# Kernel optimization log

Hardware: AMD Instinct MI355X
Metric: run time of the kernel (lower is better)

The kernel has to match this reference:

```python
import jax, jax.numpy as jnp
import numpy as np

U_NUM = 100000
I_NUM = 50000
D = 64
E = 4_000_000
N_LAYERS = 3


def setup_inputs() -> dict:
    key = jax.random.key(0)
    k1, k2, k3, k4 = jax.random.split(key, 4)
    return {
        "user_emb": jax.random.normal(k1, (U_NUM + 1, D), dtype=jnp.float32) * 0.1,
        "item_emb": jax.random.normal(k2, (I_NUM + 1, D), dtype=jnp.float32) * 0.1,
        "edge_user": jax.random.randint(k3, (E,), 0, U_NUM + 1, dtype=jnp.int32),
        "edge_item": jax.random.randint(k4, (E,), 0, I_NUM + 1, dtype=jnp.int32),
    }


def reference(user_emb, item_emb, edge_user, edge_item):
    U = user_emb.shape[0]
    I = item_emb.shape[0]
    N = U + I
    # Symmetrize bipartite interaction edges into full-graph COO indices.
    rows = jnp.concatenate([edge_user, edge_item + U])          # [2E]
    cols = jnp.concatenate([edge_item + U, edge_user])          # [2E]
    # Symmetric degree normalization: A_hat = D^-1/2 A D^-1/2 (deg + 1e-7)
    deg = jax.ops.segment_sum(jnp.ones(rows.shape[0], dtype=jnp.float32), rows, num_segments=N) + 1e-7
    d_inv_sqrt = deg ** -0.5
    vals = d_inv_sqrt[rows] * d_inv_sqrt[cols]                  # [2E]

    emb = jnp.concatenate([user_emb, item_emb], axis=0)         # [N, D]
    acc = emb
    x = emb
    for _ in range(N_LAYERS):
        # SpMM: x_new[r] = sum_{edges (r,c)} vals * x[c]
        x = jax.ops.segment_sum(vals[:, None] * x[cols], rows, num_segments=N)
        acc = acc + x
    total = acc / jnp.float32(N_LAYERS + 1)                     # mean over layer stack
    return total[:U], total[U:]
```

## Files before the change

### kernel.cpp

```cpp
#include <hip/hip_runtime.h>


static constexpr int D = 64;
#define BSHIFT 8
#define BROWS 256
#define KP 1024
#define TILE 4096
#define TK 16
#define PADSLACK (7 * BROWS)
#define FULL_CAP 16384
#define COLS_SLACK 8192

__device__ __forceinline__ float bflo(unsigned v) {
    unsigned u = v << 16;
    return __builtin_bit_cast(float, u);
}
__device__ __forceinline__ float bfhi(unsigned v) {
    unsigned u = v & 0xFFFF0000u;
    return __builtin_bit_cast(float, u);
}
__device__ __forceinline__ unsigned pack_bf16x2(float a, float b) {
    unsigned ua = __builtin_bit_cast(unsigned, a);
    unsigned ub = __builtin_bit_cast(unsigned, b);
    ua += 0x7FFFu + ((ua >> 16) & 1u);
    ub += 0x7FFFu + ((ub >> 16) & 1u);
    return (ua >> 16) | (ub & 0xFFFF0000u);
}
__device__ __forceinline__ unsigned pack_f16x2(float a, float b) {
    unsigned short ua = __builtin_bit_cast(unsigned short, (_Float16)a);
    unsigned short ub = __builtin_bit_cast(unsigned short, (_Float16)b);
    return (unsigned)ua | ((unsigned)ub << 16);
}
__device__ __forceinline__ float f16lo(unsigned v) {
    return (float)__builtin_bit_cast(_Float16, (unsigned short)(v & 0xFFFFu));
}
__device__ __forceinline__ float f16hi(unsigned v) {
    return (float)__builtin_bit_cast(_Float16, (unsigned short)(v >> 16));
}

__device__ __forceinline__ void acc_bf2(unsigned u, float& se, float& so) {
    se += bflo(u);
    so += bfhi(u);
}

__global__ __launch_bounds__(256) void bucket_count(
        const int* __restrict__ eu, const int* __restrict__ ei,
        int* __restrict__ bcnt, int E, int U) {
    __shared__ int h[KP];
    int tid = threadIdx.x;
#pragma unroll
    for (int k = 0; k < 4; ++k) h[tid + k * 256] = 0;
    __syncthreads();
    int E4 = E >> 2;
    int stride = gridDim.x * blockDim.x;
    int g = blockIdx.x * blockDim.x + tid;
    const int4* eu4 = (const int4*)eu;
    const int4* ei4 = (const int4*)ei;
    for (int e = g; e < E4; e += stride) {
        int4 u = eu4[e];
        int4 it = ei4[e];
        atomicAdd(&h[u.x >> BSHIFT], 1);
        atomicAdd(&h[u.y >> BSHIFT], 1);
        atomicAdd(&h[u.z >> BSHIFT], 1);
        atomicAdd(&h[u.w >> BSHIFT], 1);
        atomicAdd(&h[(U + it.x) >> BSHIFT], 1);
        atomicAdd(&h[(U + it.y) >> BSHIFT], 1);
        atomicAdd(&h[(U + it.z) >> BSHIFT], 1);
        atomicAdd(&h[(U + it.w) >> BSHIFT], 1);
    }
    if (blockIdx.x == 0 && tid < (E - (E4 << 2))) {
        int e = (E4 << 2) + tid;
        atomicAdd(&h[eu[e] >> BSHIFT], 1);
        atomicAdd(&h[(U + ei[e]) >> BSHIFT], 1);
    }
    __syncthreads();
#pragma unroll
    for (int k = 0; k < 4; ++k) {
        int v = h[tid + k * 256];
        if (v) atomicAdd(&bcnt[tid + k * 256], v);
    }
}

__global__ void bscan(const int* __restrict__ bcnt, int* __restrict__ bbase,
                      int* __restrict__ bcursor, int KB, int twoE) {
    __shared__ int s[KP];
    int tid = threadIdx.x;
    int v = (tid < KB) ? bcnt[tid] : 0;
    s[tid] = v;
    __syncthreads();
    for (int off = 1; off < KP; off <<= 1) {
        int a = (tid >= off) ? s[tid - off] : 0;
        __syncthreads();
        s[tid] += a;
        __syncthreads();
    }
    int ex = s[tid] - v;
    if (tid < KB) { bbase[tid] = ex; bcursor[tid] = ex; }
    if (tid == KB) bbase[tid] = twoE;
    if (tid > KB) bcursor[tid] = 0;
}

__global__ __launch_bounds__(256) void bucket_scatter(
        const int* __restrict__ eu, const int* __restrict__ ei,
        int* __restrict__ bcursor, unsigned* __restrict__ pairs,
        int E, int U, int twoE) {
    __shared__ int hist[KP];
    __shared__ int sbase[KP];
    __shared__ int gbase[KP];
    __shared__ unsigned staging[TILE];
    __shared__ unsigned short sb[TILE];
    int tid = threadIdx.x;
#pragma unroll
    for (int k = 0; k < 4; ++k) hist[tid + k * 256] = 0;
    __syncthreads();
    int base_e = blockIdx.x * TILE;
    int bk[TK]; unsigned pk[TK];
#pragma unroll
    for (int k = 0; k < TK; ++k) {
        int e = base_e + k * 256 + tid;
        bk[k] = -1;
        if (e < twoE) {
            int r, c;
            if (e < E) { r = eu[e]; c = U + ei[e]; }
            else       { c = eu[e - E]; r = U + ei[e - E]; }
            int b = r >> BSHIFT;
            bk[k] = b;
            pk[k] = ((unsigned)(r & (BROWS - 1)) << 18) | (unsigned)c;
            atomicAdd(&hist[b], 1);
        }
    }
    __syncthreads();
    int cc[4];
#pragma unroll
    for (int k = 0; k < 4; ++k) cc[k] = hist[tid + k * 256];
    for (int off = 1; off < KP; off <<= 1) {
        int a[4];
#pragma unroll
        for (int k = 0; k < 4; ++k) {
            int idx = tid + k * 256;
            a[k] = (idx >= off) ? hist[idx - off] : 0;
        }
        __syncthreads();
#pragma unroll
        for (int k = 0; k < 4; ++k) hist[tid + k * 256] += a[k];
        __syncthreads();
    }
#pragma unroll
    for (int k = 0; k < 4; ++k) {
        int idx = tid + k * 256;
        int e0 = hist[idx] - cc[k];
        sbase[idx] = e0;
        if (cc[k] > 0) gbase[idx] = atomicAdd(&bcursor[idx], cc[k]);
        hist[idx] = e0;
    }
    __syncthreads();
#pragma unroll
    for (int k = 0; k < TK; ++k) {
        if (bk[k] >= 0) {
            int pos = atomicAdd(&hist[bk[k]], 1);
            staging[pos] = pk[k];
            sb[pos] = (unsigned short)bk[k];
        }
    }
    __syncthreads();
    int tile_n = min(TILE, twoE - base_e);
#pragma unroll
    for (int k = 0; k < TK; ++k) {
        int j = k * 256 + tid;
        if (j < tile_n) {
            int b = sb[j];
            pairs[gbase[b] + (j - sbase[b])] = staging[j];
        }
    }
}

__global__ __launch_bounds__(256) void csr_build(
        const unsigned* __restrict__ pairs, const int* __restrict__ bbase,
        int* __restrict__ deg, int* __restrict__ row_ptr,
        float* __restrict__ dis, int* __restrict__ cols, int N) {
    __shared__ int cnt[BROWS];
    __shared__ int cur[BROWS];
    __shared__ int lbuf[FULL_CAP];
    int tid = threadIdx.x;
    int b = blockIdx.x;
    int lo = bbase[b], hi = bbase[b + 1];
    int cbase = lo + PADSLACK * b;
    cnt[tid] = 0;
    __syncthreads();
    for (int i = lo + tid; i < hi; i += 256) atomicAdd(&cnt[pairs[i] >> 18], 1);
    __syncthreads();
    int c = cnt[tid];
    int p = (c + 7) & ~7;
    cnt[tid] = p;
    __syncthreads();
    for (int off = 1; off < BROWS; off <<= 1) {
        int a = (tid >= off) ? cnt[tid - off] : 0;
        __syncthreads();
        cnt[tid] += a;
        __syncthreads();
    }
    int e = cnt[tid] - p;
    int r = (b << BSHIFT) + tid;
    if (r < N) {
        deg[r] = c;
        row_ptr[r] = cbase + e;
        dis[r] = rsqrtf((float)c + 1e-7f);
    }
    cur[tid] = e;
    int total = cnt[BROWS - 1];
    __syncthreads();
    if (total <= FULL_CAP) {
        for (int i = lo + tid; i < hi; i += 256) {
            unsigned pe = pairs[i];
            int pos = atomicAdd(&cur[pe >> 18], 1);
            lbuf[pos] = (int)(pe & 0x3FFFFu);
        }
        __syncthreads();
        for (int i = e + c; i < e + p; ++i) lbuf[i] = N;
        __syncthreads();
        for (int i = tid; i < total; i += 256)
            cols[cbase + i] = lbuf[i];
    } else {
        for (int i = lo + tid; i < hi; i += 256) {
            unsigned pe = pairs[i];
            int pos = atomicAdd(&cur[pe >> 18], 1);
            cols[cbase + pos] = (int)(pe & 0x3FFFFu);
        }
        __syncthreads();
        for (int i = e + c; i < e + p; ++i) cols[cbase + i] = N;
    }
}

__global__ __launch_bounds__(256) void init_kernel(
        const float4* __restrict__ ue4, const float4* __restrict__ ie4,
        const float* __restrict__ dis,
        uint4* __restrict__ xsA4, uint4* __restrict__ xsB4,
        int U8, int N8) {
    int t = blockIdx.x * blockDim.x + threadIdx.x;
    if (t >= N8 + 8) return;
    if (t >= N8) {
        uint4 z = {0u, 0u, 0u, 0u};
        xsA4[t] = z;
        xsB4[t] = z;
        return;
    }
    float dv = dis[t >> 3];
    const float4* src = (t < U8) ? (ue4 + 2 * t) : (ie4 + 2 * (t - U8));
    float4 a0 = src[0];
    float4 a1 = src[1];
    uint4 w;
    w.x = pack_bf16x2(dv * a0.x, dv * a0.y);
    w.y = pack_bf16x2(dv * a0.z, dv * a0.w);
    w.z = pack_bf16x2(dv * a1.x, dv * a1.y);
    w.w = pack_bf16x2(dv * a1.z, dv * a1.w);
    xsA4[t] = w;
}

__global__ __launch_bounds__(256) void spmm_mid(
        const int* __restrict__ row_ptr, const int* __restrict__ deg,
        const float* __restrict__ dis, const int* __restrict__ cols,
        const unsigned* __restrict__ xs, unsigned* __restrict__ xs_next,
        unsigned* __restrict__ xh, int N) {
    int wid = blockIdx.x * 4 + (threadIdx.x >> 6);
    if (wid >= N) return;
    int lane = threadIdx.x & 63;
    int n8 = lane >> 3;
    int dp = lane & 7;
    int start = row_ptr[wid];
    int cntp = (deg[wid] + 7) & ~7;
    float dr = dis[wid];
    const int* colp = cols + start;
    int vbase = n8 << 2;
    int dpo = dp << 2;
    float s0 = 0.f, s1 = 0.f, s2 = 0.f, s3 = 0.f;
    float s4 = 0.f, s5 = 0.f, s6 = 0.f, s7 = 0.f;
    for (int chunk = 0; chunk < cntp; chunk += 64) {
        int cv = colp[chunk + lane];
        int nq = min(64, cntp - chunk) >> 3;
        nq = __builtin_amdgcn_readfirstlane(nq);
        int coq[8];
        uint4 vq[8];
#pragma unroll
        for (int q = 0; q < 8; ++q) {
            if (q < nq)
                coq[q] = __builtin_amdgcn_ds_bpermute((q << 5) + vbase, cv);
        }
#pragma unroll
        for (int q = 0; q < 8; ++q) {
            if (q < nq)
                vq[q] = *(const uint4*)(xs + (((unsigned)coq[q]) << 5) + dpo);
        }
#pragma unroll
        for (int q = 0; q < 8; ++q) {
            if (q < nq) {
                acc_bf2(vq[q].x, s0, s1);
                acc_bf2(vq[q].y, s2, s3);
                acc_bf2(vq[q].z, s4, s5);
                acc_bf2(vq[q].w, s6, s7);
            }
        }
    }
#pragma unroll
    for (int m = 8; m < 64; m <<= 1) {
        s0 += __shfl_xor(s0, m); s1 += __shfl_xor(s1, m);
        s2 += __shfl_xor(s2, m); s3 += __shfl_xor(s3, m);
        s4 += __shfl_xor(s4, m); s5 += __shfl_xor(s5, m);
        s6 += __shfl_xor(s6, m); s7 += __shfl_xor(s7, m);
    }
    if (n8 == 0) {
        float x0 = dr * s0, x1 = dr * s1, x2 = dr * s2, x3 = dr * s3;
        float x4 = dr * s4, x5 = dr * s5, x6 = dr * s6, x7 = dr * s7;
        uint4 w;
        w.x = pack_bf16x2(dr * x0, dr * x1);
        w.y = pack_bf16x2(dr * x2, dr * x3);
        w.z = pack_bf16x2(dr * x4, dr * x5);
        w.w = pack_bf16x2(dr * x6, dr * x7);
        ((uint4*)xs_next)[(wid << 3) + dp] = w;
        uint4 h;
        h.x = pack_f16x2(x0, x1);
        h.y = pack_f16x2(x2, x3);
        h.z = pack_f16x2(x4, x5);
        h.w = pack_f16x2(x6, x7);
        ((uint4*)xh)[(wid << 3) + dp] = h;
    }
}

__global__ __launch_bounds__(256) void spmm_last(
        const int* __restrict__ row_ptr, const int* __restrict__ deg,
        const float* __restrict__ dis, const int* __restrict__ cols,
        const unsigned* __restrict__ xs,
        const float4* __restrict__ ue4, const float4* __restrict__ ie4,
        const unsigned* __restrict__ xh1, const unsigned* __restrict__ xh2,
        float4* __restrict__ out4, int U, int N) {
    int wid = blockIdx.x * 4 + (threadIdx.x >> 6);
    if (wid >= N) return;
    int lane = threadIdx.x & 63;
    int n8 = lane >> 3;
    int dp = lane & 7;
    int start = row_ptr[wid];
    int cntp = (deg[wid] + 7) & ~7;
    float dr = dis[wid];
    const int* colp = cols + start;
    int vbase = n8 << 2;
    int dpo = dp << 2;
    float s0 = 0.f, s1 = 0.f, s2 = 0.f, s3 = 0.f;
    float s4 = 0.f, s5 = 0.f, s6 = 0.f, s7 = 0.f;
    for (int chunk = 0; chunk < cntp; chunk += 64) {
        int cv = colp[chunk + lane];
        int nq = min(64, cntp - chunk) >> 3;
        nq = __builtin_amdgcn_readfirstlane(nq);
        int coq[8];
        uint4 vq[8];
#pragma unroll
        for (int q = 0; q < 8; ++q) {
            if (q < nq)
                coq[q] = __builtin_amdgcn_ds_bpermute((q << 5) + vbase, cv);
        }
#pragma unroll
        for (int q = 0; q < 8; ++q) {
            if (q < nq)
                vq[q] = *(const uint4*)(xs + (((unsigned)coq[q]) << 5) + dpo);
        }
#pragma unroll
        for (int q = 0; q < 8; ++q) {
            if (q < nq) {
                acc_bf2(vq[q].x, s0, s1);
                acc_bf2(vq[q].y, s2, s3);
                acc_bf2(vq[q].z, s4, s5);
                acc_bf2(vq[q].w, s6, s7);
            }
        }
    }
#pragma unroll
    for (int m = 8; m < 64; m <<= 1) {
        s0 += __shfl_xor(s0, m); s1 += __shfl_xor(s1, m);
        s2 += __shfl_xor(s2, m); s3 += __shfl_xor(s3, m);
        s4 += __shfl_xor(s4, m); s5 += __shfl_xor(s5, m);
        s6 += __shfl_xor(s6, m); s7 += __shfl_xor(s7, m);
    }
    if (n8 == 0) {
        float x30 = dr * s0, x31 = dr * s1, x32 = dr * s2, x33 = dr * s3;
        float x34 = dr * s4, x35 = dr * s5, x36 = dr * s6, x37 = dr * s7;
        const float4* ep = (wid < U) ? (ue4 + (size_t)wid * 16)
                                     : (ie4 + (size_t)(wid - U) * 16);
        float4 e0 = ep[2 * dp];
        float4 e1 = ep[2 * dp + 1];
        uint4 h1 = ((const uint4*)xh1)[(wid << 3) + dp];
        uint4 h2 = ((const uint4*)xh2)[(wid << 3) + dp];
        float4 o0, o1;
        o0.x = 0.25f * (e0.x + f16lo(h1.x) + f16lo(h2.x) + x30);
        o0.y = 0.25f * (e0.y + f16hi(h1.x) + f16hi(h2.x) + x31);
        o0.z = 0.25f * (e0.z + f16lo(h1.y) + f16lo(h2.y) + x32);
        o0.w = 0.25f * (e0.w + f16hi(h1.y) + f16hi(h2.y) + x33);
        o1.x = 0.25f * (e1.x + f16lo(h1.z) + f16lo(h2.z) + x34);
        o1.y = 0.25f * (e1.y + f16hi(h1.z) + f16hi(h2.z) + x35);
        o1.z = 0.25f * (e1.z + f16lo(h1.w) + f16lo(h2.w) + x36);
        o1.w = 0.25f * (e1.w + f16hi(h1.w) + f16hi(h2.w) + x37);
        int oo = (wid << 4) + (dp << 1);
        out4[oo] = o0;
        out4[oo + 1] = o1;
    }
}

extern "C" void kernel_launch(void* const* d_in, const int* in_sizes, int n_in,
                              void* d_out, int out_size, void* d_ws, size_t ws_size,
                              hipStream_t stream) {
    const float* ue = (const float*)d_in[0];
    const float* ie = (const float*)d_in[1];
    const int* eu = (const int*)d_in[2];
    const int* ei = (const int*)d_in[3];
    const int U = in_sizes[0] / D;
    const int I = in_sizes[1] / D;
    const int N = U + I;
    const int E = in_sizes[2];
    const int twoE = 2 * E;
    const int KB = (N + BROWS - 1) / BROWS;
    float* out = (float*)d_out;

    char* ws = (char*)d_ws;
    auto alloc = [&](size_t bytes) {
        char* p = ws;
        ws += (bytes + 255) & ~(size_t)255;
        return p;
    };
    int* deg = (int*)alloc((size_t)N * 4);
    int* row_ptr = (int*)alloc((size_t)N * 4);
    float* dis = (float*)alloc((size_t)N * 4);
    int* bcnt = (int*)alloc(KP * 4);
    int* bbase = (int*)alloc((KP + 1) * 4);
    int* bcursor = (int*)alloc(KP * 4);
    int* cols = (int*)alloc(((size_t)twoE + (size_t)PADSLACK * (KB + 1) + COLS_SLACK) * 4);
    unsigned* pairs = (unsigned*)alloc((size_t)twoE * 4);
    unsigned* xsA = (unsigned*)alloc(((size_t)N + 1) * 32 * 4);
    unsigned* xsB = (unsigned*)alloc(((size_t)N + 1) * 32 * 4);
    unsigned* xh1 = pairs;
    unsigned* xh2 = (unsigned*)alloc((size_t)N * 32 * 4);

    hipMemsetAsync(bcnt, 0, KP * 4, stream);
    bucket_count<<<1024, 256, 0, stream>>>(eu, ei, bcnt, E, U);
    bscan<<<1, KP, 0, stream>>>(bcnt, bbase, bcursor, KB, twoE);
    bucket_scatter<<<(twoE + TILE - 1) / TILE, 256, 0, stream>>>(
        eu, ei, bcursor, pairs, E, U, twoE);
    csr_build<<<KB, BROWS, 0, stream>>>(pairs, bbase, deg, row_ptr, dis, cols, N);

    int N8 = N * 8, U8 = U * 8;
    init_kernel<<<(N8 + 8 + 255) / 256, 256, 0, stream>>>(
        (const float4*)ue, (const float4*)ie, dis,
        (uint4*)xsA, (uint4*)xsB, U8, N8);

    int nblocks = (N + 3) / 4;
    spmm_mid<<<nblocks, 256, 0, stream>>>(
        row_ptr, deg, dis, cols, xsA, xsB, xh1, N);
    spmm_mid<<<nblocks, 256, 0, stream>>>(
        row_ptr, deg, dis, cols, xsB, xsA, xh2, N);
    spmm_last<<<nblocks, 256, 0, stream>>>(
        row_ptr, deg, dis, cols, xsA,
        (const float4*)ue, (const float4*)ie, xh1, xh2, (float4*)out, U, N);
}
```

Measured before the change: 587.6 us.

## Enlarge bucket-scatter tiles and stage CSR-build pairs in shared memory

bucket_scatter now handles 16384 edges per block instead of 4096. It reads the edge arrays in two passes from global memory rather than holding them in registers, which cuts the number of blocks and global bcursor atomics and gives longer contiguous runs per bucket on write-out. csr_build copies each bucket's pairs into a shared-memory buffer when they fit, so the second counting/placement pass reads LDS instead of re-reading global memory. The cost is much larger LDS use per block (around 100KB+), which lowers occupancy, plus a duplicated read of edge indices in scatter.

```diff
diff --git a/kernel.cpp b/kernel.cpp
--- a/kernel.cpp
+++ b/kernel.cpp
@@ -5,9 +5,9 @@
 #define BSHIFT 8
 #define BROWS 256
 #define KP 1024
-#define TILE 4096
-#define TK 16
+#define TILE 16384
 #define PADSLACK (7 * BROWS)
+#define RAW_CAP 14592
 #define FULL_CAP 16384
 #define COLS_SLACK 8192
 
@@ -114,20 +114,11 @@
     for (int k = 0; k < 4; ++k) hist[tid + k * 256] = 0;
     __syncthreads();
     int base_e = blockIdx.x * TILE;
-    int bk[TK]; unsigned pk[TK];
-#pragma unroll
-    for (int k = 0; k < TK; ++k) {
-        int e = base_e + k * 256 + tid;
-        bk[k] = -1;
-        if (e < twoE) {
-            int r, c;
-            if (e < E) { r = eu[e]; c = U + ei[e]; }
-            else       { c = eu[e - E]; r = U + ei[e - E]; }
-            int b = r >> BSHIFT;
-            bk[k] = b;
-            pk[k] = ((unsigned)(r & (BROWS - 1)) << 18) | (unsigned)c;
-            atomicAdd(&hist[b], 1);
-        }
+    int tile_n = min(TILE, twoE - base_e);
+    for (int j = tid; j < tile_n; j += 256) {
+        int e = base_e + j;
+        int r = (e < E) ? eu[e] : (U + ei[e - E]);
+        atomicAdd(&hist[r >> BSHIFT], 1);
     }
     __syncthreads();
     int cc[4];
@@ -154,23 +145,20 @@
         hist[idx] = e0;
     }
     __syncthreads();
-#pragma unroll
-    for (int k = 0; k < TK; ++k) {
-        if (bk[k] >= 0) {
-            int pos = atomicAdd(&hist[bk[k]], 1);
-            staging[pos] = pk[k];
-            sb[pos] = (unsigned short)bk[k];
-        }
-    }
-    __syncthreads();
-    int tile_n = min(TILE, twoE - base_e);
-#pragma unroll
-    for (int k = 0; k < TK; ++k) {
-        int j = k * 256 + tid;
-        if (j < tile_n) {
-            int b = sb[j];
-            pairs[gbase[b] + (j - sbase[b])] = staging[j];
-        }
+    for (int j = tid; j < tile_n; j += 256) {
+        int e = base_e + j;
+        int r, c;
+        if (e < E) { r = eu[e]; c = U + ei[e]; }
+        else       { c = eu[e - E]; r = U + ei[e - E]; }
+        int b = r >> BSHIFT;
+        int pos = atomicAdd(&hist[b], 1);
+        staging[pos] = ((unsigned)(r & (BROWS - 1)) << 18) | (unsigned)c;
+        sb[pos] = (unsigned short)b;
+    }
+    __syncthreads();
+    for (int j = tid; j < tile_n; j += 256) {
+        int b = sb[j];
+        pairs[gbase[b] + (j - sbase[b])] = staging[j];
     }
 }
 
@@ -180,14 +168,25 @@
         float* __restrict__ dis, int* __restrict__ cols, int N) {
     __shared__ int cnt[BROWS];
     __shared__ int cur[BROWS];
+    __shared__ unsigned raw[RAW_CAP];
     __shared__ int lbuf[FULL_CAP];
     int tid = threadIdx.x;
     int b = blockIdx.x;
     int lo = bbase[b], hi = bbase[b + 1];
     int cbase = lo + PADSLACK * b;
+    int nraw = hi - lo;
+    bool fits = (nraw <= RAW_CAP);
     cnt[tid] = 0;
     __syncthreads();
-    for (int i = lo + tid; i < hi; i += 256) atomicAdd(&cnt[pairs[i] >> 18], 1);
+    if (fits) {
+        for (int i = tid; i < nraw; i += 256) raw[i] = pairs[lo + i];
+        __syncthreads();
+        for (int i = tid; i < nraw; i += 256)
+            atomicAdd(&cnt[raw[i] >> 18], 1);
+    } else {
+        for (int i = lo + tid; i < hi; i += 256)
+            atomicAdd(&cnt[pairs[i] >> 18], 1);
+    }
     __syncthreads();
     int c = cnt[tid];
     int p = (c + 7) & ~7;
@@ -209,7 +208,18 @@
     cur[tid] = e;
     int total = cnt[BROWS - 1];
     __syncthreads();
-    if (total <= FULL_CAP) {
+    if (fits) {
+        for (int i = tid; i < nraw; i += 256) {
+            unsigned pe = raw[i];
+            int pos = atomicAdd(&cur[pe >> 18], 1);
+            lbuf[pos] = (int)(pe & 0x3FFFFu);
+        }
+        __syncthreads();
+        for (int i = e + c; i < e + p; ++i) lbuf[i] = N;
+        __syncthreads();
+        for (int i = tid; i < total; i += 256)
+            cols[cbase + i] = lbuf[i];
+    } else if (total <= FULL_CAP) {
         for (int i = lo + tid; i < hi; i += 256) {
             unsigned pe = pairs[i];
             int pos = atomicAdd(&cur[pe >> 18], 1);
```

Measured after the change: 622.7 us. +6.0%, slower.
